# Performance work log

Measured on AMD Instinct MI355X. Metric: run time of the kernel, lower is better.

## Reference

```python
import jax, jax.numpy as jnp
import numpy as np

N = 512      # n_res (act is a square pair representation [N, N, C])
C = 128      # act_dim / c_pair
I = 128      # num_intermediate_channel
EQUATION = 'ikc,jkc->ijc'  # 'outgoing' triangle multiplication
EPS = 1e-5

def _layernorm(x, g, b):
    mu = jnp.mean(x, axis=-1, keepdims=True)
    var = jnp.mean(jnp.square(x - mu), axis=-1, keepdims=True)
    return (x - mu) * jax.lax.rsqrt(var + EPS) * g + b

def setup_inputs() -> dict:
    key = jax.random.key(0)
    ks = jax.random.split(key, 12)
    s_c = 1.0 / np.sqrt(C)
    s_i = 1.0 / np.sqrt(I)
    return {
        'act': 0.1 * jax.random.normal(ks[0], (N, N, C), dtype=jnp.float32),
        'mask': (jax.random.uniform(ks[1], (N, N)) > 0.5).astype(jnp.float32),
        'ln_in_g': jnp.ones((C,), jnp.float32),
        'ln_in_b': jnp.zeros((C,), jnp.float32),
        'lp_w': s_c * jax.random.normal(ks[2], (C, I), jnp.float32),
        'lp_b': jnp.zeros((I,), jnp.float32),
        'rp_w': s_c * jax.random.normal(ks[3], (C, I), jnp.float32),
        'rp_b': jnp.zeros((I,), jnp.float32),
        'lg_w': s_c * jax.random.normal(ks[4], (C, I), jnp.float32),
        'lg_b': jnp.zeros((I,), jnp.float32),
        'rg_w': s_c * jax.random.normal(ks[5], (C, I), jnp.float32),
        'rg_b': jnp.zeros((I,), jnp.float32),
        'ln_c_g': jnp.ones((I,), jnp.float32),
        'ln_c_b': jnp.zeros((I,), jnp.float32),
        'out_w': s_i * jax.random.normal(ks[6], (I, C), jnp.float32),
        'out_b': jnp.zeros((C,), jnp.float32),
        'gate_w': s_c * jax.random.normal(ks[7], (C, C), jnp.float32),
        'gate_b': jnp.zeros((C,), jnp.float32),
    }

def reference(act, mask, ln_in_g, ln_in_b, lp_w, lp_b, rp_w, rp_b,
              lg_w, lg_b, rg_w, rg_b, ln_c_g, ln_c_b, out_w, out_b,
              gate_w, gate_b):
    m = mask[..., None]                                   # [N, N, 1]
    a = _layernorm(act, ln_in_g, ln_in_b)                 # input layernorm
    input_act = a
    # masked projections fused with sigmoid gates
    left = m * (a @ lp_w + lp_b) * jax.nn.sigmoid(a @ lg_w + lg_b)    # [N,N,I]
    right = m * (a @ rp_w + rp_b) * jax.nn.sigmoid(a @ rg_w + rg_b)   # [N,N,I]
    # triangle update: per-channel [N,N] x [N,N]^T matmul
    x = jnp.einsum(EQUATION, left, right)                 # [N,N,I]
    x = _layernorm(x, ln_c_g, ln_c_b)
    gate = jax.nn.sigmoid(input_act @ gate_w + gate_b)    # [N,N,C]
    return (x @ out_w + out_b) * gate
```

## Files before the change

### kernel.cpp

```cpp
#include <hip/hip_runtime.h>

#define NRES 512
#define N2   262144

typedef __attribute__((ext_vector_type(8))) short s16x8;
typedef __attribute__((ext_vector_type(4))) float f32x4;

__device__ __forceinline__ ushort f2bf(float x){
  union { float f; unsigned u; } v; v.f = x;
  unsigned r = (v.u + 0x7FFFu + ((v.u >> 16) & 1u)) >> 16;
  return (ushort)r;
}
__device__ __forceinline__ float bf2f(ushort h){
  union { unsigned u; float f; } v; v.u = ((unsigned)h) << 16; return v.f;
}
__device__ __forceinline__ float sigm(float x){ return 1.0f / (1.0f + __expf(-x)); }

__device__ __forceinline__ void gld_lds16(const void* g, void* lds){
  __builtin_amdgcn_global_load_lds((const __attribute__((address_space(1))) void*)g,
                                   (__attribute__((address_space(3))) void*)lds, 16, 0, 0);
}

__global__ void k0_prep(const float* __restrict__ lp, const float* __restrict__ lg,
                        const float* __restrict__ rp, const float* __restrict__ rg,
                        const float* __restrict__ gw, const float* __restrict__ ow,
                        ushort* __restrict__ Wt)
{
  const float* srcs[6] = {lp, lg, rp, rg, gw, ow};
  const float* wsrc = srcs[blockIdx.x];
  ushort* dst = Wt + blockIdx.x * 16384;
  for (int f = threadIdx.x; f < 16384; f += blockDim.x){
    int n = f >> 7, k = f & 127;
    dst[f] = f2bf(wsrc[k * 128 + n]);
  }
}

__device__ __forceinline__ void stage_w(const ushort* __restrict__ Wt_m,
                                        ushort* Wlds, int t)
{
  #pragma unroll
  for (int u = 0; u < 8; ++u){
    int f = t + u * 256;
    int n = f >> 4, k8 = f & 15;
    *(s16x8*)&Wlds[n * 136 + k8 * 8] = *(const s16x8*)(Wt_m + f * 8);
  }
}

__device__ __forceinline__ void do_gemm128(const ushort* Alds, const ushort* Wlds,
                                           int wr, int wc, int cl, int h,
                                           f32x4 acc[4][4])
{
  #pragma unroll
  for (int ks = 0; ks < 4; ++ks){
    s16x8 a[4], b[4];
    #pragma unroll
    for (int m = 0; m < 4; ++m)
      a[m] = *(const s16x8*)&Alds[(wr*64 + m*16 + cl) * 136 + ks*32 + h*8];
    #pragma unroll
    for (int n = 0; n < 4; ++n)
      b[n] = *(const s16x8*)&Wlds[(wc*64 + n*16 + cl) * 136 + ks*32 + h*8];
    #pragma unroll
    for (int m = 0; m < 4; ++m)
      #pragma unroll
      for (int n = 0; n < 4; ++n)
        acc[m][n] = __builtin_amdgcn_mfma_f32_16x16x32_bf16(a[m], b[n], acc[m][n], 0, 0, 0);
  }
}

__global__ __launch_bounds__(256) void k1_proj(
    const float* __restrict__ act,  const float* __restrict__ mask,
    const float* __restrict__ ln_g, const float* __restrict__ ln_b,
    const float* __restrict__ lp_b, const float* __restrict__ lg_b,
    const float* __restrict__ rp_b, const float* __restrict__ rg_b,
    const float* __restrict__ gate_b, const ushort* __restrict__ Wt,
    ushort* __restrict__ leftg, ushort* __restrict__ rightg,
    ushort* __restrict__ gateg)
{
  __shared__ ushort Alds[128 * 136];
  __shared__ ushort Wlds[128 * 136];
  const int t  = threadIdx.x;
  const int p0 = blockIdx.x * 128;

  {
    const int g = t >> 5, j = t & 31;
    const float4 gv = *(const float4*)(ln_g + j * 4);
    const float4 bv = *(const float4*)(ln_b + j * 4);
    #pragma unroll
    for (int i = 0; i < 16; ++i){
      const int r = g + (i << 3);
      float4 v = *(const float4*)(act + (size_t)(p0 + r) * 128 + j * 4);
      float s = v.x + v.y + v.z + v.w;
      float q = v.x*v.x + v.y*v.y + v.z*v.z + v.w*v.w;
      #pragma unroll
      for (int m = 1; m < 32; m <<= 1){ s += __shfl_xor(s, m); q += __shfl_xor(q, m); }
      float mu = s * (1.0f / 128.0f);
      float rs = rsqrtf(q * (1.0f / 128.0f) - mu * mu + 1e-5f);
      ushort4 o;
      o.x = f2bf((v.x - mu) * rs * gv.x + bv.x);
      o.y = f2bf((v.y - mu) * rs * gv.y + bv.y);
      o.z = f2bf((v.z - mu) * rs * gv.z + bv.z);
      o.w = f2bf((v.w - mu) * rs * gv.w + bv.w);
      *(ushort4*)&Alds[r * 136 + j * 4] = o;
    }
  }
  __syncthreads();

  const int lane = t & 63, w = t >> 6;
  const int wr = w >> 1, wc = w & 1;
  const int cl = lane & 15, h = lane >> 4;

  f32x4 accP[4][4], accG[4][4];
  const f32x4 z = {0.f, 0.f, 0.f, 0.f};

  const float* pbias[2] = {lp_b, rp_b};
  const float* gbias[2] = {lg_b, rg_b};
  ushort* dsts[2] = {leftg, rightg};

  for (int grp = 0; grp < 2; ++grp){
    const int s0 = grp * 2;
    stage_w(Wt + (size_t)s0 * 16384, Wlds, t);
    __syncthreads();
    #pragma unroll
    for (int m = 0; m < 4; ++m)
      #pragma unroll
      for (int n = 0; n < 4; ++n) accP[m][n] = z;
    do_gemm128(Alds, Wlds, wr, wc, cl, h, accP);
    __syncthreads();
    stage_w(Wt + (size_t)(s0 + 1) * 16384, Wlds, t);
    __syncthreads();
    #pragma unroll
    for (int m = 0; m < 4; ++m)
      #pragma unroll
      for (int n = 0; n < 4; ++n) accG[m][n] = z;
    do_gemm128(Alds, Wlds, wr, wc, cl, h, accG);
    __syncthreads();

    float mk[4][4];
    #pragma unroll
    for (int m = 0; m < 4; ++m)
      #pragma unroll
      for (int r = 0; r < 4; ++r)
        mk[m][r] = mask[p0 + wr*64 + m*16 + h*4 + r];
    float pb[4], gb[4];
    #pragma unroll
    for (int n = 0; n < 4; ++n){
      int c = wc*64 + n*16 + cl;
      pb[n] = pbias[grp][c];
      gb[n] = gbias[grp][c];
    }
    #pragma unroll
    for (int m = 0; m < 4; ++m)
      #pragma unroll
      for (int n = 0; n < 4; ++n){
        int c = wc*64 + n*16 + cl;
        #pragma unroll
        for (int r = 0; r < 4; ++r){
          int pl = wr*64 + m*16 + h*4 + r;
          float val = mk[m][r] * (accP[m][n][r] + pb[n]) * sigm(accG[m][n][r] + gb[n]);
          Wlds[c * 136 + pl] = f2bf(val);
        }
      }
    __syncthreads();
    ushort* dst = dsts[grp];
    #pragma unroll
    for (int u = 0; u < 8; ++u){
      int f = t + u * 256;
      int c = f >> 4, p8 = f & 15;
      *(s16x8*)(dst + (size_t)c * N2 + p0 + p8 * 8) =
          *(const s16x8*)&Wlds[c * 136 + p8 * 8];
    }
    __syncthreads();
  }

  stage_w(Wt + (size_t)4 * 16384, Wlds, t);
  __syncthreads();
  #pragma unroll
  for (int m = 0; m < 4; ++m)
    #pragma unroll
    for (int n = 0; n < 4; ++n) accP[m][n] = z;
  do_gemm128(Alds, Wlds, wr, wc, cl, h, accP);
  __syncthreads();
  {
    float gbv[4];
    #pragma unroll
    for (int n = 0; n < 4; ++n) gbv[n] = gate_b[wc*64 + n*16 + cl];
    #pragma unroll
    for (int m = 0; m < 4; ++m)
      #pragma unroll
      for (int n = 0; n < 4; ++n){
        int c = wc*64 + n*16 + cl;
        #pragma unroll
        for (int r = 0; r < 4; ++r){
          int pl = wr*64 + m*16 + h*4 + r;
          Wlds[pl * 136 + c] = f2bf(sigm(accP[m][n][r] + gbv[n]));
        }
      }
  }
  __syncthreads();
  #pragma unroll
  for (int u = 0; u < 8; ++u){
    int f = t + u * 256;
    int p = f >> 4, c8 = f & 15;
    *(s16x8*)(gateg + (size_t)(p0 + p) * 128 + c8 * 8) =
        *(const s16x8*)&Wlds[p * 136 + c8 * 8];
  }
}

__global__ __launch_bounds__(256) void k2_tri(const ushort* __restrict__ leftg,
                                              const ushort* __restrict__ rightg,
                                              float* __restrict__ X)
{
  __shared__ ushort Ab[128 * 32];
  __shared__ ushort Bb[128 * 32];
  const int t = threadIdx.x, lane = t & 63, w = t >> 6;
  const int b = blockIdx.x;
  const int c = b & 127, tile = b >> 7;
  const int tm = (tile >> 2) * 128, tn = (tile & 3) * 128;
  const ushort* Lc = leftg  + (size_t)c * N2;
  const ushort* Rc = rightg + (size_t)c * N2;
  float* Xc = X + (size_t)c * N2;
  const int wr = w >> 1, wc = w & 1, cl = lane & 15, h = lane >> 4;

  f32x4 acc[4][4];
  const f32x4 z = {0.f, 0.f, 0.f, 0.f};
  #pragma unroll
  for (int m = 0; m < 4; ++m)
    #pragma unroll
    for (int n = 0; n < 4; ++n) acc[m][n] = z;

  for (int kt = 0; kt < 16; ++kt){
    __syncthreads();
    #pragma unroll
    for (int s = 0; s < 2; ++s){
      const int q = w + 4 * s;
      const int o = q * 1024 + lane * 16;
      const int row = o >> 6, kb = o & 63;
      gld_lds16((const char*)Lc + (size_t)(tm + row) * 1024 + kt * 64 + kb,
                (char*)Ab + q * 1024);
      gld_lds16((const char*)Rc + (size_t)(tn + row) * 1024 + kt * 64 + kb,
                (char*)Bb + q * 1024);
    }
    __syncthreads();
    s16x8 a[4], bf[4];
    #pragma unroll
    for (int m = 0; m < 4; ++m)
      a[m] = *(const s16x8*)&Ab[(wr*64 + m*16 + cl) * 32 + h * 8];
    #pragma unroll
    for (int n = 0; n < 4; ++n)
      bf[n] = *(const s16x8*)&Bb[(wc*64 + n*16 + cl) * 32 + h * 8];
    #pragma unroll
    for (int m = 0; m < 4; ++m)
      #pragma unroll
      for (int n = 0; n < 4; ++n)
        acc[m][n] = __builtin_amdgcn_mfma_f32_16x16x32_bf16(a[m], bf[n], acc[m][n], 0, 0, 0);
  }

  #pragma unroll
  for (int m = 0; m < 4; ++m)
    #pragma unroll
    for (int n = 0; n < 4; ++n)
      #pragma unroll
      for (int r = 0; r < 4; ++r)
        Xc[(size_t)(tm + wr*64 + m*16 + h*4 + r) * NRES + tn + wc*64 + n*16 + cl] =
            acc[m][n][r];
}

__global__ __launch_bounds__(256) void k3_out(
    const float* __restrict__ X, const ushort* __restrict__ gateg,
    const ushort* __restrict__ Wt5,
    const float* __restrict__ ln_g, const float* __restrict__ ln_b,
    const float* __restrict__ ob, float* __restrict__ out)
{
  __shared__ ushort Alds[128 * 136];
  __shared__ ushort Wlds[128 * 136];
  __shared__ float part[8][2][128];
  __shared__ float stat[2][128];
  const int t = threadIdx.x;
  const int p0 = blockIdx.x * 128;
  const int g = t >> 5, j = t & 31;

  float4 xv[16];
  float s0 = 0, s1 = 0, s2 = 0, s3 = 0, q0 = 0, q1 = 0, q2 = 0, q3 = 0;
  #pragma unroll
  for (int i = 0; i < 16; ++i){
    const int cch = g + (i << 3);
    xv[i] = *(const float4*)(X + (size_t)cch * N2 + p0 + j * 4);
    s0 += xv[i].x; q0 += xv[i].x * xv[i].x;
    s1 += xv[i].y; q1 += xv[i].y * xv[i].y;
    s2 += xv[i].z; q2 += xv[i].z * xv[i].z;
    s3 += xv[i].w; q3 += xv[i].w * xv[i].w;
  }
  part[g][0][j*4+0] = s0; part[g][0][j*4+1] = s1;
  part[g][0][j*4+2] = s2; part[g][0][j*4+3] = s3;
  part[g][1][j*4+0] = q0; part[g][1][j*4+1] = q1;
  part[g][1][j*4+2] = q2; part[g][1][j*4+3] = q3;
  __syncthreads();
  if (t < 128){
    float s = 0, q = 0;
    #pragma unroll
    for (int gg = 0; gg < 8; ++gg){ s += part[gg][0][t]; q += part[gg][1][t]; }
    float mu = s * (1.0f / 128.0f);
    float rs = rsqrtf(q * (1.0f / 128.0f) - mu * mu + 1e-5f);
    stat[0][t] = mu; stat[1][t] = rs;
  }
  __syncthreads();
  #pragma unroll
  for (int i = 0; i < 16; ++i){
    const int cch = g + (i << 3);
    const float gc = ln_g[cch], bc = ln_b[cch];
    const int p = j * 4;
    Alds[(p+0) * 136 + cch] = f2bf((xv[i].x - stat[0][p+0]) * stat[1][p+0] * gc + bc);
    Alds[(p+1) * 136 + cch] = f2bf((xv[i].y - stat[0][p+1]) * stat[1][p+1] * gc + bc);
    Alds[(p+2) * 136 + cch] = f2bf((xv[i].z - stat[0][p+2]) * stat[1][p+2] * gc + bc);
    Alds[(p+3) * 136 + cch] = f2bf((xv[i].w - stat[0][p+3]) * stat[1][p+3] * gc + bc);
  }
  stage_w(Wt5, Wlds, t);
  __syncthreads();

  const int lane = t & 63, w = t >> 6;
  const int wr = w >> 1, wc = w & 1, cl = lane & 15, h = lane >> 4;
  f32x4 acc[4][4];
  const f32x4 z = {0.f, 0.f, 0.f, 0.f};
  #pragma unroll
  for (int m = 0; m < 4; ++m)
    #pragma unroll
    for (int n = 0; n < 4; ++n) acc[m][n] = z;
  do_gemm128(Alds, Wlds, wr, wc, cl, h, acc);

  float obv[4];
  #pragma unroll
  for (int n = 0; n < 4; ++n) obv[n] = ob[wc*64 + n*16 + cl];
  #pragma unroll
  for (int m = 0; m < 4; ++m)
    #pragma unroll
    for (int n = 0; n < 4; ++n){
      const int cc = wc*64 + n*16 + cl;
      #pragma unroll
      for (int r = 0; r < 4; ++r){
        const size_t p = p0 + wr*64 + m*16 + h*4 + r;
        out[p * 128 + cc] = (acc[m][n][r] + obv[n]) * bf2f(gateg[p * 128 + cc]);
      }
    }
}

extern "C" void kernel_launch(void* const* d_in, const int* in_sizes, int n_in,
                              void* d_out, int out_size, void* d_ws, size_t ws_size,
                              hipStream_t stream)
{
  const float* act    = (const float*)d_in[0];
  const float* mask   = (const float*)d_in[1];
  const float* ln_in_g = (const float*)d_in[2];
  const float* ln_in_b = (const float*)d_in[3];
  const float* lp_w = (const float*)d_in[4];
  const float* lp_b = (const float*)d_in[5];
  const float* rp_w = (const float*)d_in[6];
  const float* rp_b = (const float*)d_in[7];
  const float* lg_w = (const float*)d_in[8];
  const float* lg_b = (const float*)d_in[9];
  const float* rg_w = (const float*)d_in[10];
  const float* rg_b = (const float*)d_in[11];
  const float* ln_c_g = (const float*)d_in[12];
  const float* ln_c_b = (const float*)d_in[13];
  const float* out_w  = (const float*)d_in[14];
  const float* out_b  = (const float*)d_in[15];
  const float* gate_w = (const float*)d_in[16];
  const float* gate_b = (const float*)d_in[17];
  float* outp = (float*)d_out;

  char* ws = (char*)d_ws;
  ushort* Wt     = (ushort*)(ws);
  ushort* leftg  = (ushort*)(ws + 196608);
  ushort* rightg = (ushort*)(ws + 196608 + 67108864ull);
  ushort* gateg  = (ushort*)(ws + 196608 + 2ull * 67108864ull);
  float*  X      = (float*) (ws + 196608 + 3ull * 67108864ull);

  k0_prep<<<dim3(6), dim3(256), 0, stream>>>(lp_w, lg_w, rp_w, rg_w, gate_w, out_w, Wt);
  k1_proj<<<dim3(2048), dim3(256), 0, stream>>>(act, mask, ln_in_g, ln_in_b,
                                                lp_b, lg_b, rp_b, rg_b, gate_b,
                                                Wt, leftg, rightg, gateg);
  k2_tri<<<dim3(2048), dim3(256), 0, stream>>>(leftg, rightg, X);
  k3_out<<<dim3(2048), dim3(256), 0, stream>>>(X, gateg, Wt + 5 * 16384,
                                               ln_c_g, ln_c_b, out_b, outp);
}
```

Baseline: 605.1 us.

## Restructure projection kernel to read weights from global memory into registers

The projection kernel no longer stages each 128x128 weight matrix into LDS with block-wide barriers. Each wave now holds A fragments in registers for a 64-row half and loads its 32-column weight slices straight from global/L2 into registers. Projection and gate matmuls are interleaved, and the masked gated outputs go directly to global as 8-byte stores. The gate output uses a small per-wave LDS scratch for coalesced row writes. This removes most __syncthreads and the large Wlds buffer, which may raise occupancy, but it adds uncached-in-LDS weight reloads per wave and narrower, less coalesced channel-major stores.

After: 580.5 us. 4.1% less time.

```diff
diff --git a/kernel.cpp b/kernel.cpp
--- a/kernel.cpp
+++ b/kernel.cpp
@@ -32,38 +32,6 @@
   for (int f = threadIdx.x; f < 16384; f += blockDim.x){
     int n = f >> 7, k = f & 127;
     dst[f] = f2bf(wsrc[k * 128 + n]);
-  }
-}
-
-__device__ __forceinline__ void stage_w(const ushort* __restrict__ Wt_m,
-                                        ushort* Wlds, int t)
-{
-  #pragma unroll
-  for (int u = 0; u < 8; ++u){
-    int f = t + u * 256;
-    int n = f >> 4, k8 = f & 15;
-    *(s16x8*)&Wlds[n * 136 + k8 * 8] = *(const s16x8*)(Wt_m + f * 8);
-  }
-}
-
-__device__ __forceinline__ void do_gemm128(const ushort* Alds, const ushort* Wlds,
-                                           int wr, int wc, int cl, int h,
-                                           f32x4 acc[4][4])
-{
-  #pragma unroll
-  for (int ks = 0; ks < 4; ++ks){
-    s16x8 a[4], b[4];
-    #pragma unroll
-    for (int m = 0; m < 4; ++m)
-      a[m] = *(const s16x8*)&Alds[(wr*64 + m*16 + cl) * 136 + ks*32 + h*8];
-    #pragma unroll
-    for (int n = 0; n < 4; ++n)
-      b[n] = *(const s16x8*)&Wlds[(wc*64 + n*16 + cl) * 136 + ks*32 + h*8];
-    #pragma unroll
-    for (int m = 0; m < 4; ++m)
-      #pragma unroll
-      for (int n = 0; n < 4; ++n)
-        acc[m][n] = __builtin_amdgcn_mfma_f32_16x16x32_bf16(a[m], b[n], acc[m][n], 0, 0, 0);
   }
 }
 
@@ -77,7 +45,7 @@
     ushort* __restrict__ gateg)
 {
   __shared__ ushort Alds[128 * 136];
-  __shared__ ushort Wlds[128 * 136];
+  __shared__ ushort Gscr[4][64 * 32];
   const int t  = threadIdx.x;
   const int p0 = blockIdx.x * 128;
 
@@ -106,103 +74,96 @@
   __syncthreads();
 
   const int lane = t & 63, w = t >> 6;
-  const int wr = w >> 1, wc = w & 1;
   const int cl = lane & 15, h = lane >> 4;
-
-  f32x4 accP[4][4], accG[4][4];
   const f32x4 z = {0.f, 0.f, 0.f, 0.f};
 
   const float* pbias[2] = {lp_b, rp_b};
   const float* gbias[2] = {lg_b, rg_b};
   ushort* dsts[2] = {leftg, rightg};
 
-  for (int grp = 0; grp < 2; ++grp){
-    const int s0 = grp * 2;
-    stage_w(Wt + (size_t)s0 * 16384, Wlds, t);
-    __syncthreads();
-    #pragma unroll
-    for (int m = 0; m < 4; ++m)
-      #pragma unroll
-      for (int n = 0; n < 4; ++n) accP[m][n] = z;
-    do_gemm128(Alds, Wlds, wr, wc, cl, h, accP);
-    __syncthreads();
-    stage_w(Wt + (size_t)(s0 + 1) * 16384, Wlds, t);
-    __syncthreads();
-    #pragma unroll
-    for (int m = 0; m < 4; ++m)
-      #pragma unroll
-      for (int n = 0; n < 4; ++n) accG[m][n] = z;
-    do_gemm128(Alds, Wlds, wr, wc, cl, h, accG);
-    __syncthreads();
+  for (int mh = 0; mh < 2; ++mh){
+    s16x8 a[4][4];
+    #pragma unroll
+    for (int m = 0; m < 4; ++m)
+      #pragma unroll
+      for (int ks = 0; ks < 4; ++ks)
+        a[m][ks] = *(const s16x8*)&Alds[(mh*64 + m*16 + cl) * 136 + ks*32 + h*8];
 
     float mk[4][4];
     #pragma unroll
     for (int m = 0; m < 4; ++m)
       #pragma unroll
       for (int r = 0; r < 4; ++r)
-        mk[m][r] = mask[p0 + wr*64 + m*16 + h*4 + r];
-    float pb[4], gb[4];
-    #pragma unroll
-    for (int n = 0; n < 4; ++n){
-      int c = wc*64 + n*16 + cl;
-      pb[n] = pbias[grp][c];
-      gb[n] = gbias[grp][c];
-    }
-    #pragma unroll
-    for (int m = 0; m < 4; ++m)
-      #pragma unroll
-      for (int n = 0; n < 4; ++n){
-        int c = wc*64 + n*16 + cl;
-        #pragma unroll
-        for (int r = 0; r < 4; ++r){
-          int pl = wr*64 + m*16 + h*4 + r;
-          float val = mk[m][r] * (accP[m][n][r] + pb[n]) * sigm(accG[m][n][r] + gb[n]);
-          Wlds[c * 136 + pl] = f2bf(val);
+        mk[m][r] = mask[p0 + mh*64 + m*16 + h*4 + r];
+
+    #pragma unroll
+    for (int grp = 0; grp < 2; ++grp){
+      ushort* dst = dsts[grp];
+      #pragma unroll
+      for (int rep = 0; rep < 2; ++rep){
+        const int c0 = (w * 2 + rep) * 16;
+        const ushort* WP = Wt + (size_t)(grp * 2) * 16384 + (size_t)(c0 + cl) * 128;
+        const ushort* WG = WP + 16384;
+        s16x8 bP[4], bG[4];
+        #pragma unroll
+        for (int ks = 0; ks < 4; ++ks){
+          bP[ks] = *(const s16x8*)(WP + ks*32 + h*8);
+          bG[ks] = *(const s16x8*)(WG + ks*32 + h*8);
+        }
+        f32x4 accP[4], accG[4];
+        #pragma unroll
+        for (int m = 0; m < 4; ++m){ accP[m] = z; accG[m] = z; }
+        #pragma unroll
+        for (int ks = 0; ks < 4; ++ks)
+          #pragma unroll
+          for (int m = 0; m < 4; ++m){
+            accP[m] = __builtin_amdgcn_mfma_f32_16x16x32_bf16(a[m][ks], bP[ks], accP[m], 0, 0, 0);
+            accG[m] = __builtin_amdgcn_mfma_f32_16x16x32_bf16(a[m][ks], bG[ks], accG[m], 0, 0, 0);
+          }
+        const float pb = pbias[grp][c0 + cl];
+        const float gb = gbias[grp][c0 + cl];
+        #pragma unroll
+        for (int m = 0; m < 4; ++m){
+          ushort4 o;
+          o.x = f2bf(mk[m][0] * (accP[m][0] + pb) * sigm(accG[m][0] + gb));
+          o.y = f2bf(mk[m][1] * (accP[m][1] + pb) * sigm(accG[m][1] + gb));
+          o.z = f2bf(mk[m][2] * (accP[m][2] + pb) * sigm(accG[m][2] + gb));
+          o.w = f2bf(mk[m][3] * (accP[m][3] + pb) * sigm(accG[m][3] + gb));
+          *(ushort4*)(dst + (size_t)(c0 + cl) * N2 + p0 + mh*64 + m*16 + h*4) = o;
         }
       }
-    __syncthreads();
-    ushort* dst = dsts[grp];
-    #pragma unroll
-    for (int u = 0; u < 8; ++u){
-      int f = t + u * 256;
-      int c = f >> 4, p8 = f & 15;
-      *(s16x8*)(dst + (size_t)c * N2 + p0 + p8 * 8) =
-          *(const s16x8*)&Wlds[c * 136 + p8 * 8];
-    }
-    __syncthreads();
-  }
-
-  stage_w(Wt + (size_t)4 * 16384, Wlds, t);
-  __syncthreads();
-  #pragma unroll
-  for (int m = 0; m < 4; ++m)
-    #pragma unroll
-    for (int n = 0; n < 4; ++n) accP[m][n] = z;
-  do_gemm128(Alds, Wlds, wr, wc, cl, h, accP);
-  __syncthreads();
-  {
-    float gbv[4];
-    #pragma unroll
-    for (int n = 0; n < 4; ++n) gbv[n] = gate_b[wc*64 + n*16 + cl];
-    #pragma unroll
-    for (int m = 0; m < 4; ++m)
-      #pragma unroll
-      for (int n = 0; n < 4; ++n){
-        int c = wc*64 + n*16 + cl;
-        #pragma unroll
-        for (int r = 0; r < 4; ++r){
-          int pl = wr*64 + m*16 + h*4 + r;
-          Wlds[pl * 136 + c] = f2bf(sigm(accP[m][n][r] + gbv[n]));
-        }
-      }
-  }
-  __syncthreads();
-  #pragma unroll
-  for (int u = 0; u < 8; ++u){
-    int f = t + u * 256;
-    int p = f >> 4, c8 = f & 15;
-    *(s16x8*)(gateg + (size_t)(p0 + p) * 128 + c8 * 8) =
-        *(const s16x8*)&Wlds[p * 136 + c8 * 8];
+    }
+
+    #pragma unroll
+    for (int rep = 0; rep < 2; ++rep){
+      const int c0 = (w * 2 + rep) * 16;
+      const ushort* W5 = Wt + (size_t)4 * 16384 + (size_t)(c0 + cl) * 128;
+      s16x8 b[4];
+      #pragma unroll
+      for (int ks = 0; ks < 4; ++ks)
+        b[ks] = *(const s16x8*)(W5 + ks*32 + h*8);
+      f32x4 acc[4];
+      #pragma unroll
+      for (int m = 0; m < 4; ++m) acc[m] = z;
+      #pragma unroll
+      for (int ks = 0; ks < 4; ++ks)
+        #pragma unroll
+        for (int m = 0; m < 4; ++m)
+          acc[m] = __builtin_amdgcn_mfma_f32_16x16x32_bf16(a[m][ks], b[ks], acc[m], 0, 0, 0);
+      const float gbv = gate_b[c0 + cl];
+      #pragma unroll
+      for (int m = 0; m < 4; ++m)
+        #pragma unroll
+        for (int r = 0; r < 4; ++r)
+          Gscr[w][(m*16 + h*4 + r) * 32 + rep*16 + cl] = f2bf(sigm(acc[m][r] + gbv));
+    }
+    #pragma unroll
+    for (int u = 0; u < 4; ++u){
+      const int f = u * 64 + lane;
+      const int p = f >> 2, ci = f & 3;
+      *(s16x8*)(gateg + (size_t)(p0 + mh*64 + p) * 128 + w*32 + ci*8) =
+          *(const s16x8*)&Gscr[w][p*32 + ci*8];
+    }
   }
 }
 
@@ -314,7 +275,14 @@
     Alds[(p+2) * 136 + cch] = f2bf((xv[i].z - stat[0][p+2]) * stat[1][p+2] * gc + bc);
     Alds[(p+3) * 136 + cch] = f2bf((xv[i].w - stat[0][p+3]) * stat[1][p+3] * gc + bc);
   }
-  stage_w(Wt5, Wlds, t);
+  {
+    #pragma unroll
+    for (int u = 0; u < 8; ++u){
+      int f = t + u * 256;
+      int n = f >> 4, k8 = f & 15;
+      *(s16x8*)&Wlds[n * 136 + k8 * 8] = *(const s16x8*)(Wt5 + f * 8);
+    }
+  }
   __syncthreads();
 
   const int lane = t & 63, w = t >> 6;
@@ -325,7 +293,21 @@
   for (int m = 0; m < 4; ++m)
     #pragma unroll
     for (int n = 0; n < 4; ++n) acc[m][n] = z;
-  do_gemm128(Alds, Wlds, wr, wc, cl, h, acc);
+  #pragma unroll
+  for (int ks = 0; ks < 4; ++ks){
+    s16x8 a[4], b[4];
+    #pragma unroll
+    for (int m = 0; m < 4; ++m)
+      a[m] = *(const s16x8*)&Alds[(wr*64 + m*16 + cl) * 136 + ks*32 + h*8];
+    #pragma unroll
+    for (int n = 0; n < 4; ++n)
+      b[n] = *(const s16x8*)&Wlds[(wc*64 + n*16 + cl) * 136 + ks*32 + h*8];
+    #pragma unroll
+    for (int m = 0; m < 4; ++m)
+      #pragma unroll
+      for (int n = 0; n < 4; ++n)
+        acc[m][n] = __builtin_amdgcn_mfma_f32_16x16x32_bf16(a[m], b[n], acc[m][n], 0, 0, 0);
+  }
 
   float obv[4];
   #pragma unroll
```
